# Kernel optimization log

Measured on AMD Instinct MI355X. Metric: run time of the kernel, lower is better.

The kernel has to match this reference:

```python
import jax, jax.numpy as jnp
import numpy as np

H = 128  # hidden size (fixed in module)


def _lstm(x, W_ih, W_hh, b_ih, b_hh):
    # x: [T, B, I]; PyTorch gate order: i, f, g, o
    T, B, _ = x.shape
    # precompute input contribution for all timesteps: [T, B, 4H]
    xg = jnp.einsum('tbi,gi->tbg', x, W_ih) + b_ih + b_hh
    h0 = jnp.zeros((B, H), x.dtype)
    c0 = jnp.zeros((B, H), x.dtype)

    def step(carry, xg_t):
        h, c = carry
        gates = xg_t + h @ W_hh.T  # [B, 4H]
        i = jax.nn.sigmoid(gates[:, 0 * H:1 * H])
        f = jax.nn.sigmoid(gates[:, 1 * H:2 * H])
        g = jnp.tanh(gates[:, 2 * H:3 * H])
        o = jax.nn.sigmoid(gates[:, 3 * H:4 * H])
        c = f * c + i * g
        h = o * jnp.tanh(c)
        return (h, c), h

    _, out = jax.lax.scan(step, (h0, c0), xg)  # out: [T, B, H]
    return out


def setup_inputs() -> dict:
    key = jax.random.key(0)
    ks = jax.random.split(key, 7)
    T, B, I = 1024, 512, 13
    s = 1.0 / np.sqrt(H)
    return {
        'x': jax.random.normal(ks[0], (T, B, I), jnp.float32),
        'W_ih': jax.random.uniform(ks[1], (4 * H, I), jnp.float32, -s, s),
        'W_hh': jax.random.uniform(ks[2], (4 * H, H), jnp.float32, -s, s),
        'b_ih': jax.random.uniform(ks[3], (4 * H,), jnp.float32, -s, s),
        'b_hh': jax.random.uniform(ks[4], (4 * H,), jnp.float32, -s, s),
        'W_fc': jax.random.uniform(ks[5], (7, H), jnp.float32, -s, s),
        'b_fc': jax.random.uniform(ks[6], (7,), jnp.float32, -s, s),
    }


def reference(x, W_ih, W_hh, b_ih, b_hh, W_fc, b_fc):
    out = _lstm(x, W_ih, W_hh, b_ih, b_hh)        # [T, B, H]
    logits = out.reshape(-1, H) @ W_fc.T + b_fc    # [T*B, 7]
    return jax.nn.softmax(logits, axis=1)
```

## Files before the change

### kernel.cpp

```cpp
#include <hip/hip_runtime.h>

#define H_ 128
#define T_ 1024
#define B_ 512
#define I_ 13
#define LOG2E 1.4426950408889634f

typedef _Float16 half8 __attribute__((ext_vector_type(8)));
typedef float float4_ __attribute__((ext_vector_type(4)));

static __device__ __forceinline__ float fast_rcp(float v) {
  return __builtin_amdgcn_rcpf(v);
}
static __device__ __forceinline__ float fast_exp2(float v) {
  return __builtin_amdgcn_exp2f(v);
}
static __device__ __forceinline__ float sigmoid_f(float v) {
  return fast_rcp(1.0f + fast_exp2(-LOG2E * v));
}
static __device__ __forceinline__ float tanh_f(float v) {
  return 2.0f * fast_rcp(1.0f + fast_exp2(-2.0f * LOG2E * v)) - 1.0f;
}

__global__ __launch_bounds__(512, 1) void lstm_fused(
    const float* __restrict__ x, const float* __restrict__ Wih,
    const float* __restrict__ Whh, const float* __restrict__ bih,
    const float* __restrict__ bhh, const float* __restrict__ Wfc,
    const float* __restrict__ bfc, float* __restrict__ out)
{
  __shared__ __align__(16) _Float16 xlds[T_][2][16];
  __shared__ __align__(16) float lgring[T_][2][8];
  __shared__ __align__(16) _Float16 abuf[2][2][168];

  const int tid  = threadIdx.x;
  const int wave = tid >> 6;
  const int lane = tid & 63;
  const int n16  = lane & 15;
  const int quad = lane >> 4;
  const int wgb  = blockIdx.x * 2;

  half8 wfrag[4][5];
  float biasv[4];
  #pragma unroll
  for (int ti = 0; ti < 4; ++ti) {
    const int tile = ti * 8 + wave;
    const int col  = tile * 16 + n16;
    biasv[ti] = bih[col] + bhh[col];
    #pragma unroll
    for (int kc = 0; kc < 5; ++kc) {
      half8 f;
      #pragma unroll
      for (int j = 0; j < 8; ++j) {
        const int k = kc * 32 + quad * 8 + j;
        float v = 0.0f;
        if (k < 128)            v = Whh[col * H_ + k];
        else if (k < 128 + I_)  v = Wih[col * I_ + (k - 128)];
        f[j] = (_Float16)v;
      }
      wfrag[ti][kc] = f;
    }
  }
  half8 wfc[4];
  const float biasfc = (n16 < 7) ? bfc[n16] : 0.0f;
  #pragma unroll
  for (int kc = 0; kc < 4; ++kc) {
    half8 f;
    #pragma unroll
    for (int j = 0; j < 8; ++j) {
      const int k = kc * 32 + quad * 8 + j;
      f[j] = (_Float16)((n16 < 7) ? Wfc[n16 * H_ + k] : 0.0f);
    }
    wfc[kc] = f;
  }

  for (int idx = tid; idx < T_ * 2 * 16; idx += 512) {
    const int t  = idx >> 5;
    const int rw = (idx >> 4) & 1;
    const int ii = idx & 15;
    float v = 0.0f;
    if (ii < I_) v = x[((size_t)t * B_ + wgb + rw) * I_ + ii];
    xlds[t][rw][ii] = (_Float16)v;
  }
  for (int idx = tid; idx < 2 * 2 * 168; idx += 512)
    ((_Float16*)abuf)[idx] = (_Float16)0.0f;
  __syncthreads();

  float c_state = 0.0f;
  const bool aload = (n16 & 3) == 0;
  const int  arow  = (n16 >> 2) & 1;

  half8 af[4];
  half8 af4;
  {
    half8 z;
    #pragma unroll
    for (int j = 0; j < 8; ++j) z[j] = (_Float16)0.0f;
    #pragma unroll
    for (int kc = 0; kc < 4; ++kc) af[kc] = z;
    af4 = z;
  }
  if (aload && quad < 2)
    af4 = *(const half8*)&xlds[0][arow][quad * 8];

  float4_ acc[4];
  #pragma unroll
  for (int ti = 0; ti < 4; ++ti)
    #pragma unroll
    for (int r = 0; r < 4; ++r) acc[ti][r] = 0.0f;
  float4_ accf;
  #pragma unroll
  for (int r = 0; r < 4; ++r) accf[r] = 0.0f;

  #pragma unroll
  for (int ti = 0; ti < 4; ++ti) acc[ti][0] = biasv[ti];
  #pragma unroll
  for (int ti = 0; ti < 4; ++ti)
    acc[ti] = __builtin_amdgcn_mfma_f32_16x16x32_f16(af4, wfrag[ti][4], acc[ti], 0, 0, 0);

  for (int t = 0; t <= T_; ++t) {
    if (aload) {
      #pragma unroll
      for (int kc = 0; kc < 4; ++kc)
        af[kc] = *(const half8*)&abuf[t & 1][arow][kc * 32 + quad * 8];
    }

    if (wave == 7 && t >= 1) {
      accf[0] = biasfc;
      #pragma unroll
      for (int kc = 0; kc < 4; ++kc)
        accf = __builtin_amdgcn_mfma_f32_16x16x32_f16(af[kc], wfc[kc], accf, 0, 0, 0);
      if (lane < 32 && n16 < 7)
        lgring[t - 1][quad][n16] = accf[0];
    }

    if (t < T_) {
      #pragma unroll
      for (int kc = 0; kc < 4; ++kc) {
        #pragma unroll
        for (int ti = 0; ti < 4; ++ti)
          acc[ti] = __builtin_amdgcn_mfma_f32_16x16x32_f16(af[kc], wfrag[ti][kc], acc[ti], 0, 0, 0);
      }

      if (aload && quad < 2 && t + 1 < T_)
        af4 = *(const half8*)&xlds[t + 1][arow][quad * 8];

      const float iv = sigmoid_f(acc[0][0]);
      const float fv = sigmoid_f(acc[1][0]);
      const float gg = tanh_f(acc[2][0]);
      const float ov = sigmoid_f(acc[3][0]);
      c_state = fv * c_state + iv * gg;
      const float hv = ov * tanh_f(c_state);
      if (lane < 32)
        abuf[(t + 1) & 1][quad][16 * wave + n16] = (_Float16)hv;

      #pragma unroll
      for (int ti = 0; ti < 4; ++ti) acc[ti][0] = biasv[ti];
      #pragma unroll
      for (int ti = 0; ti < 4; ++ti)
        acc[ti] = __builtin_amdgcn_mfma_f32_16x16x32_f16(af4, wfrag[ti][4], acc[ti], 0, 0, 0);
    }

    __syncthreads();
  }

  for (int r = tid; r < T_ * 2; r += 512) {
    const int t = r >> 1;
    const int b = r & 1;
    float lg[7];
    float mx = -3.0e38f;
    #pragma unroll
    for (int k = 0; k < 7; ++k) {
      lg[k] = lgring[t][b][k];
      mx = fmaxf(mx, lg[k]);
    }
    float s = 0.0f;
    #pragma unroll
    for (int k = 0; k < 7; ++k) {
      lg[k] = fast_exp2(LOG2E * (lg[k] - mx));
      s += lg[k];
    }
    const float rs = fast_rcp(s);
    float* op = &out[((size_t)t * B_ + wgb + b) * 7];
    #pragma unroll
    for (int k = 0; k < 7; ++k) op[k] = lg[k] * rs;
  }
}

extern "C" void kernel_launch(void* const* d_in, const int* in_sizes, int n_in,
                              void* d_out, int out_size, void* d_ws, size_t ws_size,
                              hipStream_t stream) {
  (void)in_sizes; (void)n_in; (void)out_size; (void)d_ws; (void)ws_size;
  const float* x   = (const float*)d_in[0];
  const float* Wih = (const float*)d_in[1];
  const float* Whh = (const float*)d_in[2];
  const float* bih = (const float*)d_in[3];
  const float* bhh = (const float*)d_in[4];
  const float* Wfc = (const float*)d_in[5];
  const float* bfc = (const float*)d_in[6];
  hipLaunchKernelGGL(lstm_fused, dim3(256), dim3(512), 0, stream,
                     x, Wih, Whh, bih, bhh, Wfc, bfc, (float*)d_out);
}
```

Before: 615.5 us.

## Split FC head across four waves and reorder gate MFMAs to overlap activations

The output-projection MFMA chain, which used to run on wave 7 alone, is now spread over waves 0-3. Each of these waves computes one K-chunk and accumulates into the LDS logits ring with shared-memory atomicAdd, and the ring is pre-initialised with the FC bias. The per-step gate MFMAs are reordered so the i and g gates finish first and their sigmoid/tanh can overlap the f and o MFMAs. The input-projection MFMAs for f and o are also moved to the top of the next step. The aim is to shorten the serial critical path of each timestep, and the cost is LDS atomics and extra initialisation work.

New measurement: 2.296 ms. 3.73x slower.

```diff
diff --git a/kernel.cpp b/kernel.cpp
--- a/kernel.cpp
+++ b/kernel.cpp
@@ -60,17 +60,16 @@
       wfrag[ti][kc] = f;
     }
   }
-  half8 wfc[4];
-  const float biasfc = (n16 < 7) ? bfc[n16] : 0.0f;
-  #pragma unroll
-  for (int kc = 0; kc < 4; ++kc) {
+  half8 wfcw;
+  {
+    const int kcw = wave & 3;
     half8 f;
     #pragma unroll
     for (int j = 0; j < 8; ++j) {
-      const int k = kc * 32 + quad * 8 + j;
+      const int k = kcw * 32 + quad * 8 + j;
       f[j] = (_Float16)((n16 < 7) ? Wfc[n16 * H_ + k] : 0.0f);
     }
-    wfc[kc] = f;
+    wfcw = f;
   }
 
   for (int idx = tid; idx < T_ * 2 * 16; idx += 512) {
@@ -81,6 +80,12 @@
     if (ii < I_) v = x[((size_t)t * B_ + wgb + rw) * I_ + ii];
     xlds[t][rw][ii] = (_Float16)v;
   }
+  for (int idx = tid; idx < T_ * 2 * 8; idx += 512) {
+    const int t = idx >> 4;
+    const int b = (idx >> 3) & 1;
+    const int k = idx & 7;
+    lgring[t][b][k] = (k < 7) ? bfc[k] : 0.0f;
+  }
   for (int idx = tid; idx < 2 * 2 * 168; idx += 512)
     ((_Float16*)abuf)[idx] = (_Float16)0.0f;
   __syncthreads();
@@ -107,15 +112,11 @@
   for (int ti = 0; ti < 4; ++ti)
     #pragma unroll
     for (int r = 0; r < 4; ++r) acc[ti][r] = 0.0f;
-  float4_ accf;
-  #pragma unroll
-  for (int r = 0; r < 4; ++r) accf[r] = 0.0f;
-
-  #pragma unroll
-  for (int ti = 0; ti < 4; ++ti) acc[ti][0] = biasv[ti];
-  #pragma unroll
-  for (int ti = 0; ti < 4; ++ti)
-    acc[ti] = __builtin_amdgcn_mfma_f32_16x16x32_f16(af4, wfrag[ti][4], acc[ti], 0, 0, 0);
+
+  acc[0][0] = biasv[0];
+  acc[2][0] = biasv[2];
+  acc[0] = __builtin_amdgcn_mfma_f32_16x16x32_f16(af4, wfrag[0][4], acc[0], 0, 0, 0);
+  acc[2] = __builtin_amdgcn_mfma_f32_16x16x32_f16(af4, wfrag[2][4], acc[2], 0, 0, 0);
 
   for (int t = 0; t <= T_; ++t) {
     if (aload) {
@@ -124,40 +125,50 @@
         af[kc] = *(const half8*)&abuf[t & 1][arow][kc * 32 + quad * 8];
     }
 
-    if (wave == 7 && t >= 1) {
-      accf[0] = biasfc;
-      #pragma unroll
-      for (int kc = 0; kc < 4; ++kc)
-        accf = __builtin_amdgcn_mfma_f32_16x16x32_f16(af[kc], wfc[kc], accf, 0, 0, 0);
+    if (t < T_) {
+      acc[1][0] = biasv[1];
+      acc[3][0] = biasv[3];
+      acc[1] = __builtin_amdgcn_mfma_f32_16x16x32_f16(af4, wfrag[1][4], acc[1], 0, 0, 0);
+      acc[3] = __builtin_amdgcn_mfma_f32_16x16x32_f16(af4, wfrag[3][4], acc[3], 0, 0, 0);
+    }
+
+    if (wave < 4 && t >= 1) {
+      float4_ accf;
+      #pragma unroll
+      for (int r = 0; r < 4; ++r) accf[r] = 0.0f;
+      accf = __builtin_amdgcn_mfma_f32_16x16x32_f16(af[wave], wfcw, accf, 0, 0, 0);
       if (lane < 32 && n16 < 7)
-        lgring[t - 1][quad][n16] = accf[0];
+        atomicAdd(&lgring[t - 1][quad][n16], accf[0]);
     }
 
     if (t < T_) {
       #pragma unroll
       for (int kc = 0; kc < 4; ++kc) {
-        #pragma unroll
-        for (int ti = 0; ti < 4; ++ti)
-          acc[ti] = __builtin_amdgcn_mfma_f32_16x16x32_f16(af[kc], wfrag[ti][kc], acc[ti], 0, 0, 0);
+        acc[0] = __builtin_amdgcn_mfma_f32_16x16x32_f16(af[kc], wfrag[0][kc], acc[0], 0, 0, 0);
+        acc[2] = __builtin_amdgcn_mfma_f32_16x16x32_f16(af[kc], wfrag[2][kc], acc[2], 0, 0, 0);
+      }
+      const float iv = sigmoid_f(acc[0][0]);
+      const float gg = tanh_f(acc[2][0]);
+      #pragma unroll
+      for (int kc = 0; kc < 4; ++kc) {
+        acc[1] = __builtin_amdgcn_mfma_f32_16x16x32_f16(af[kc], wfrag[1][kc], acc[1], 0, 0, 0);
+        acc[3] = __builtin_amdgcn_mfma_f32_16x16x32_f16(af[kc], wfrag[3][kc], acc[3], 0, 0, 0);
       }
 
       if (aload && quad < 2 && t + 1 < T_)
         af4 = *(const half8*)&xlds[t + 1][arow][quad * 8];
 
-      const float iv = sigmoid_f(acc[0][0]);
       const float fv = sigmoid_f(acc[1][0]);
-      const float gg = tanh_f(acc[2][0]);
       const float ov = sigmoid_f(acc[3][0]);
       c_state = fv * c_state + iv * gg;
       const float hv = ov * tanh_f(c_state);
       if (lane < 32)
         abuf[(t + 1) & 1][quad][16 * wave + n16] = (_Float16)hv;
 
-      #pragma unroll
-      for (int ti = 0; ti < 4; ++ti) acc[ti][0] = biasv[ti];
-      #pragma unroll
-      for (int ti = 0; ti < 4; ++ti)
-        acc[ti] = __builtin_amdgcn_mfma_f32_16x16x32_f16(af4, wfrag[ti][4], acc[ti], 0, 0, 0);
+      acc[0][0] = biasv[0];
+      acc[2][0] = biasv[2];
+      acc[0] = __builtin_amdgcn_mfma_f32_16x16x32_f16(af4, wfrag[0][4], acc[0], 0, 0, 0);
+      acc[2] = __builtin_amdgcn_mfma_f32_16x16x32_f16(af4, wfrag[2][4], acc[2], 0, 0, 0);
     }
 
     __syncthreads();
```
